# Kernel tuning notes

Measured on AMD Instinct MI355X. Metric: run time of the kernel, lower is better.

## Reference

```python
import jax, jax.numpy as jnp
import numpy as np

B, S, D = 1, 2048, 2048
H, KV, HD = 32, 8, 64  # heads, kv heads, head_dim
THETA = 10000.0


def rot(x):
    # torch: cat(-x[..., d/2:], x[..., :d/2])
    f, s = jnp.split(x, 2, axis=-1)
    return jnp.concatenate((-s, f), axis=-1)


def setup_inputs() -> dict:
    key = jax.random.key(0)
    k0, k1, k2, k3, k4 = jax.random.split(key, 5)
    x = jax.random.normal(k0, (B, S, D), jnp.float32)
    Wq = jax.random.normal(k1, (H * HD, D), jnp.float32) * 0.02
    Wk = jax.random.normal(k2, (KV * HD, D), jnp.float32) * 0.02
    Wv = jax.random.normal(k3, (KV * HD, D), jnp.float32) * 0.02
    Wo = jax.random.normal(k4, (D, H * HD), jnp.float32) * 0.02
    inv_freq = 1.0 / (THETA ** (jnp.arange(0, HD, 2, dtype=jnp.float32) / HD))
    return {"x": x, "Wq": Wq, "Wk": Wk, "Wv": Wv, "Wo": Wo, "inv_freq": inv_freq}


def reference(x, Wq, Wk, Wv, Wo, inv_freq):
    bsz, seqlen, _ = x.shape
    q = (x @ Wq.T).reshape(bsz, seqlen, H, HD).transpose(0, 2, 1, 3)   # [B,H,S,hd]
    k = (x @ Wk.T).reshape(bsz, seqlen, KV, HD).transpose(0, 2, 1, 3)  # [B,KV,S,hd]
    v = (x @ Wv.T).reshape(bsz, seqlen, KV, HD).transpose(0, 2, 1, 3)

    # RoPE cos/sin (computed under no_grad in torch)
    pos = jnp.arange(seqlen, dtype=jnp.float32)
    freqs = pos[:, None] * inv_freq[None, :]                # [S, hd/2]
    emb = jnp.concatenate((freqs, freqs), axis=-1)          # [S, hd]
    cos = jnp.cos(emb)[None, None]                          # [1,1,S,hd]
    sin = jnp.sin(emb)[None, None]
    q = q * cos + rot(q) * sin
    k = k * cos + rot(k) * sin

    # GQA: group query heads per kv head instead of repeat_interleaving kv
    G = H // KV
    qg = q.reshape(bsz, KV, G, seqlen, HD)
    scores = jnp.einsum('bkgsd,bktd->bkgst', qg, k) / jnp.sqrt(jnp.float32(HD))
    mask = jnp.triu(jnp.full((seqlen, seqlen), -jnp.inf, jnp.float32), 1)
    attn = jax.nn.softmax(scores + mask, axis=-1)
    out = jnp.einsum('bkgst,bktd->bkgsd', attn, v)          # [B,KV,G,S,hd]
    out = out.reshape(bsz, H, seqlen, HD).transpose(0, 2, 1, 3).reshape(bsz, seqlen, H * HD)
    return out @ Wo.T
```

## Files before the change

### kernel.cpp

```cpp
#include <hip/hip_runtime.h>
#include <hip/hip_bf16.h>
#include <math.h>

#define S_LEN 2048
#define D_MODEL 2048
#define N_H 32
#define N_KV 8
#define HD 64

typedef __attribute__((ext_vector_type(8))) short short8;
typedef __attribute__((ext_vector_type(4))) float floatx4;
typedef unsigned short u16;
typedef unsigned int u32;

#define QSCALE 0.18033688011112042f

#if defined(__has_builtin)
#if __has_builtin(__builtin_amdgcn_exp2f)
#define EXP2(x) __builtin_amdgcn_exp2f(x)
#else
#define EXP2(x) __expf(0.6931471805599453f * (x))
#endif
#else
#define EXP2(x) __expf(0.6931471805599453f * (x))
#endif

__device__ __forceinline__ u16 f2bf(float f) {
    union { float f; u32 u; } v; v.f = f;
    u32 r = v.u + 0x7fffu + ((v.u >> 16) & 1u);
    return (u16)(r >> 16);
}

__device__ __forceinline__ void gload16(const void* gp, void* lp) {
    __builtin_amdgcn_global_load_lds(
        (const __attribute__((address_space(1))) unsigned int*)gp,
        (__attribute__((address_space(3))) unsigned int*)lp,
        16, 0, 0);
}

__global__ __launch_bounds__(256) void cast_all(const float* __restrict__ x,
                                                const float* __restrict__ Wq,
                                                const float* __restrict__ Wk,
                                                const float* __restrict__ Wv,
                                                const float* __restrict__ Wo,
                                                const float* __restrict__ inv_freq,
                                                u16* __restrict__ xb,
                                                u16* __restrict__ wqkv,
                                                u16* __restrict__ wob,
                                                float2* __restrict__ tab) {
    const int t0 = blockIdx.x * 256 + threadIdx.x;
#pragma unroll
    for (int j = 0; j < 7; ++j) {
        const int c = t0 + j * 524288;
        const int i = c * 4;
        const int row = i >> 11;
        const int col = i & 2047;
        const float* src;
        u16* dst;
        if (row < 2048)      { src = x  + (size_t)row * 2048 + col;          dst = xb + i; }
        else if (row < 4096) { src = Wq + (size_t)(row - 2048) * 2048 + col; dst = wqkv + (i - 2048 * 2048); }
        else if (row < 4608) { src = Wk + (size_t)(row - 4096) * 2048 + col; dst = wqkv + (i - 2048 * 2048); }
        else if (row < 5120) { src = Wv + (size_t)(row - 4608) * 2048 + col; dst = wqkv + (i - 2048 * 2048); }
        else                 { src = Wo + (size_t)(row - 5120) * 2048 + col; dst = wob + (i - 5120 * 2048); }
        const float4 v = *(const float4*)src;
        ushort4 o;
        o.x = f2bf(v.x); o.y = f2bf(v.y); o.z = f2bf(v.z); o.w = f2bf(v.w);
        *(ushort4*)dst = o;
    }
    if (t0 < 65536) {
        const int s = t0 >> 5, d = t0 & 31;
        float sn, cs;
        sincosf((float)s * inv_freq[d], &sn, &cs);
        tab[t0] = make_float2(cs, sn);
    }
}

__global__ __launch_bounds__(256) void gemm_qkv(const u16* __restrict__ A,
                                                const u16* __restrict__ B,
                                                u16* __restrict__ Qh,
                                                u16* __restrict__ Kh,
                                                u16* __restrict__ Vt,
                                                const float2* __restrict__ tab,
                                                int K) {
    __shared__ u16 As[2][64 * 32];
    __shared__ u16 Bs[2][128 * 32];
    const int tid  = threadIdx.x;
    const int w    = tid >> 6;
    const int lane = tid & 63;
    const int lr   = lane & 15;
    const int quad = lane >> 4;
    const int bm = blockIdx.x * 64, bn = blockIdx.y * 128;
    const int wm = (w & 1) * 32, wn = (w >> 1) * 64;

    const int srow = tid >> 2;
    const int sch  = (tid & 3) * 8;
    const u16* Ag = A + (size_t)(bm + srow) * K + sch;
    const u16* Bg = B + (size_t)(bn + srow) * K + sch;
    const int loff = srow * 32 + sch;
    const size_t gstride = (size_t)64 * K;

    floatx4 acc[2][4];
#pragma unroll
    for (int i = 0; i < 2; ++i)
#pragma unroll
        for (int j = 0; j < 4; ++j) acc[i][j] = floatx4{0.f, 0.f, 0.f, 0.f};

    gload16(Ag, &As[0][loff]);
    gload16(Bg, &Bs[0][loff]);
    gload16(Bg + gstride, &Bs[0][loff + 64 * 32]);
    __syncthreads();

    for (int k0 = 0; k0 < K; k0 += 32) {
        const int cur = (k0 >> 5) & 1;
        if (k0 + 32 < K) {
            gload16(Ag + k0 + 32, &As[cur ^ 1][loff]);
            gload16(Bg + k0 + 32, &Bs[cur ^ 1][loff]);
            gload16(Bg + gstride + k0 + 32, &Bs[cur ^ 1][loff + 64 * 32]);
        }
        short8 af[2], bf[4];
#pragma unroll
        for (int t = 0; t < 2; ++t)
            af[t] = *(const short8*)&As[cur][(wm + t * 16 + lr) * 32 + quad * 8];
#pragma unroll
        for (int t = 0; t < 4; ++t)
            bf[t] = *(const short8*)&Bs[cur][(wn + t * 16 + lr) * 32 + quad * 8];
#pragma unroll
        for (int im = 0; im < 2; ++im)
#pragma unroll
            for (int in = 0; in < 4; ++in)
                acc[im][in] = __builtin_amdgcn_mfma_f32_16x16x32_bf16(
                    af[im], bf[in], acc[im][in], 0, 0, 0);
        __syncthreads();
    }

    const int c0 = bn + wn;
    if (bn < 2048) {
        const int h = c0 >> 6;
#pragma unroll
        for (int p = 0; p < 2; ++p) {
            const int d = p * 16 + lr;
#pragma unroll
            for (int im = 0; im < 2; ++im)
#pragma unroll
                for (int r = 0; r < 4; ++r) {
                    const int s = bm + wm + im * 16 + quad * 4 + r;
                    const float2 t = tab[s * 32 + d];
                    const float cs = t.x, sn = t.y;
                    const float xl = acc[im][p][r], xh = acc[im][p + 2][r];
                    u16* qrow = Qh + ((size_t)h * S_LEN + s) * HD;
                    qrow[d]      = f2bf((xl * cs - xh * sn) * QSCALE);
                    qrow[d + 32] = f2bf((xh * cs + xl * sn) * QSCALE);
                }
        }
    } else if (bn < 2560) {
        const int kv = (c0 - 2048) >> 6;
#pragma unroll
        for (int p = 0; p < 2; ++p) {
            const int d = p * 16 + lr;
#pragma unroll
            for (int im = 0; im < 2; ++im)
#pragma unroll
                for (int r = 0; r < 4; ++r) {
                    const int s = bm + wm + im * 16 + quad * 4 + r;
                    const float2 t = tab[s * 32 + d];
                    const float cs = t.x, sn = t.y;
                    const float xl = acc[im][p][r], xh = acc[im][p + 2][r];
                    u16* krow = Kh + ((size_t)kv * S_LEN + s) * HD;
                    krow[d]      = f2bf(xl * cs - xh * sn);
                    krow[d + 32] = f2bf(xh * cs + xl * sn);
                }
        }
    } else {
        const int kv = (c0 - 2560) >> 6;
#pragma unroll
        for (int im = 0; im < 2; ++im)
#pragma unroll
            for (int in = 0; in < 4; ++in) {
                const int dfull = in * 16 + lr;
                const int s0 = bm + wm + im * 16 + quad * 4;
                ushort4 o;
                o.x = f2bf(acc[im][in][0]); o.y = f2bf(acc[im][in][1]);
                o.z = f2bf(acc[im][in][2]); o.w = f2bf(acc[im][in][3]);
                *(ushort4*)&Vt[((size_t)kv * HD + dfull) * S_LEN + s0] = o;
            }
    }
}

__global__ __launch_bounds__(256) void gemm_out(const u16* __restrict__ A,
                                                const u16* __restrict__ B,
                                                float* __restrict__ Cf,
                                                int N, int K) {
    __shared__ u16 As[2][64 * 64];
    __shared__ u16 Bs[2][64 * 64];
    const int tid  = threadIdx.x;
    const int w    = tid >> 6;
    const int lane = tid & 63;
    const int lr   = lane & 15;
    const int quad = lane >> 4;
    const int bm = blockIdx.x * 64, bn = blockIdx.y * 64;
    const int wm = w * 16;

    const int srow = tid >> 3;
    const int sch  = tid & 7;

    floatx4 acc[4];
#pragma unroll
    for (int j = 0; j < 4; ++j) acc[j] = floatx4{0.f, 0.f, 0.f, 0.f};

#pragma unroll
    for (int j = 0; j < 2; ++j) {
        const int r = j * 32 + srow;
        gload16(A + (size_t)(bm + r) * K + ((sch ^ (r & 7)) * 8),
                &As[0][r * 64 + sch * 8]);
        gload16(B + (size_t)(bn + r) * K + ((sch ^ (r & 7)) * 8),
                &Bs[0][r * 64 + sch * 8]);
    }
    __syncthreads();

    for (int k0 = 0; k0 < K; k0 += 64) {
        const int cur = (k0 >> 6) & 1;
        if (k0 + 64 < K) {
            const int nb = cur ^ 1;
#pragma unroll
            for (int j = 0; j < 2; ++j) {
                const int r = j * 32 + srow;
                gload16(A + (size_t)(bm + r) * K + k0 + 64 + ((sch ^ (r & 7)) * 8),
                        &As[nb][r * 64 + sch * 8]);
                gload16(B + (size_t)(bn + r) * K + k0 + 64 + ((sch ^ (r & 7)) * 8),
                        &Bs[nb][r * 64 + sch * 8]);
            }
        }
#pragma unroll
        for (int kk = 0; kk < 2; ++kk) {
            short8 af, bf[4];
            {
                const int row = wm + lr;
                const int c   = kk * 4 + quad;
                af = *(const short8*)&As[cur][row * 64 + ((c ^ (row & 7)) * 8)];
            }
#pragma unroll
            for (int in = 0; in < 4; ++in) {
                const int row = in * 16 + lr;
                const int c   = kk * 4 + quad;
                bf[in] = *(const short8*)&Bs[cur][row * 64 + ((c ^ (row & 7)) * 8)];
            }
#pragma unroll
            for (int in = 0; in < 4; ++in)
                acc[in] = __builtin_amdgcn_mfma_f32_16x16x32_bf16(
                    af, bf[in], acc[in], 0, 0, 0);
        }
        __syncthreads();
    }

#pragma unroll
    for (int in = 0; in < 4; ++in) {
        const int row0 = bm + wm + quad * 4;
        const int col  = bn + in * 16 + lr;
#pragma unroll
        for (int r = 0; r < 4; ++r)
            Cf[(size_t)(row0 + r) * N + col] = acc[in][r];
    }
}

__global__ __launch_bounds__(256) void attn_mfma(const u16* __restrict__ Qh,
                                                 const u16* __restrict__ Kh,
                                                 const u16* __restrict__ Vt,
                                                 u16* __restrict__ AO) {
    __shared__ u16 QPs[64 * 64];
    __shared__ u16 Ks[2][64 * 64];
    __shared__ u16 Vs[2][64 * 64];

    const int bid = blockIdx.x;
    const int h   = bid & 31;
    const int qb  = 31 - (bid >> 5);
    const int kv  = h >> 2;
    const int tid  = threadIdx.x;
    const int w    = tid >> 6;
    const int lr   = tid & 15;
    const int quad = (tid >> 4) & 3;
    const int grow = tid >> 3;
    const int gp   = tid & 7;

    const u16* Qg = Qh + ((size_t)h * S_LEN + (size_t)qb * 64) * HD;
    const u16* Kg = Kh + (size_t)kv * S_LEN * HD;
    const u16* Vg = Vt + (size_t)kv * HD * S_LEN;

#pragma unroll
    for (int j = 0; j < 2; ++j) {
        const int r = j * 32 + grow;
        gload16(Qg + (size_t)r * HD + ((gp ^ (r & 7)) * 8), QPs + r * 64 + gp * 8);
        gload16(Kg + (size_t)r * HD + ((gp ^ (r & 7)) * 8), &Ks[0][r * 64 + gp * 8]);
        gload16(Vg + (size_t)r * S_LEN + ((gp ^ (r & 7)) * 8), &Vs[0][r * 64 + gp * 8]);
    }
    __syncthreads();

    const int wq0 = qb * 64 + w * 16;

    short8 qf[2];
#pragma unroll
    for (int kh = 0; kh < 2; ++kh) {
        const int row = w * 16 + lr;
        const int c   = kh * 4 + quad;
        qf[kh] = *(const short8*)&QPs[row * 64 + ((c ^ (row & 7)) * 8)];
    }

    const int q1  = quad >> 1;
    const int lr7 = lr & 7;
    const int pwbase = (w * 16 + lr) * 64 + (quad & 1) * 4;

    float l_lane = 0.f;
    floatx4 oacc[4];
#pragma unroll
    for (int dn = 0; dn < 4; ++dn) oacc[dn] = floatx4{0.f, 0.f, 0.f, 0.f};

    for (int kt = 0; kt <= qb; ++kt) {
        const int buf = kt & 1;
        if (kt < qb) {
            const int nb = buf ^ 1;
#pragma unroll
            for (int j = 0; j < 2; ++j) {
                const int r = j * 32 + grow;
                gload16(Kg + (size_t)((kt + 1) * 64 + r) * HD + ((gp ^ (r & 7)) * 8),
                        &Ks[nb][r * 64 + gp * 8]);
                gload16(Vg + (size_t)r * S_LEN + (kt + 1) * 64 + ((gp ^ (r & 7)) * 8),
                        &Vs[nb][r * 64 + gp * 8]);
            }
        }
        if (64 * kt <= wq0 + 15) {
            floatx4 st[4];
#pragma unroll
            for (int in = 0; in < 4; ++in) st[in] = floatx4{0.f, 0.f, 0.f, 0.f};
#pragma unroll
            for (int in = 0; in < 4; ++in)
#pragma unroll
                for (int kh = 0; kh < 2; ++kh) {
                    const int row = in * 16 + lr;
                    const int c   = kh * 4 + quad;
                    const short8 kf = *(const short8*)
                        &Ks[buf][row * 64 + ((c ^ (row & 7)) * 8)];
                    st[in] = __builtin_amdgcn_mfma_f32_16x16x32_bf16(
                        kf, qf[kh], st[in], 0, 0, 0);
                }

            const bool need_mask = (kt * 64 + 63) > wq0;
            const int qglob = wq0 + lr;
#pragma unroll
            for (int in = 0; in < 4; ++in)
#pragma unroll
                for (int r = 0; r < 4; ++r) {
                    float s = st[in][r];
                    if (need_mask) {
                        const int kg = kt * 64 + in * 16 + quad * 4 + r;
                        if (kg > qglob) s = -1e30f;
                    }
                    const float p = EXP2(s);
                    st[in][r] = p;
                    l_lane += p;
                }

#pragma unroll
            for (int in = 0; in < 4; ++in) {
                const int chunk = (((in * 2 + q1) ^ lr7) << 3);
                float2 lo2; lo2.x = st[in][0]; lo2.y = st[in][1];
                float2 hi2; hi2.x = st[in][2]; hi2.y = st[in][3];
                __hip_bfloat162 blo = __float22bfloat162_rn(lo2);
                __hip_bfloat162 bhi = __float22bfloat162_rn(hi2);
                *(u32*)&QPs[pwbase + chunk]     = *(u32*)&blo;
                *(u32*)&QPs[pwbase + chunk + 2] = *(u32*)&bhi;
            }

#pragma unroll
            for (int kc = 0; kc < 2; ++kc) {
                const int prow = w * 16 + lr;
                const short8 pf = *(const short8*)
                    &QPs[prow * 64 + (((kc * 4 + quad) ^ (prow & 7)) * 8)];
#pragma unroll
                for (int dn = 0; dn < 4; ++dn) {
                    const int vrow = dn * 16 + lr;
                    const int c    = kc * 4 + quad;
                    const short8 vf = *(const short8*)
                        &Vs[buf][vrow * 64 + ((c ^ (vrow & 7)) * 8)];
                    oacc[dn] = __builtin_amdgcn_mfma_f32_16x16x32_bf16(
                        pf, vf, oacc[dn], 0, 0, 0);
                }
            }
        }
        __syncthreads();
    }

    float lv = l_lane;
    lv += __shfl_xor(lv, 16);
    lv += __shfl_xor(lv, 32);
#pragma unroll
    for (int r = 0; r < 4; ++r) {
        const float inv = 1.f / __shfl(lv, quad * 4 + r);
        const size_t row = (size_t)(wq0 + quad * 4 + r);
#pragma unroll
        for (int dn = 0; dn < 4; ++dn)
            AO[row * D_MODEL + h * 64 + dn * 16 + lr] =
                f2bf(oacc[dn][r] * inv);
    }
}

extern "C" void kernel_launch(void* const* d_in, const int* in_sizes, int n_in,
                              void* d_out, int out_size, void* d_ws, size_t ws_size,
                              hipStream_t stream) {
    const float* x        = (const float*)d_in[0];
    const float* Wq       = (const float*)d_in[1];
    const float* Wk       = (const float*)d_in[2];
    const float* Wv       = (const float*)d_in[3];
    const float* Wo       = (const float*)d_in[4];
    const float* inv_freq = (const float*)d_in[5];
    float* out = (float*)d_out;

    const size_t ME = 1 << 20;
    u16* xb   = (u16*)d_ws;
    u16* wqkv = xb   + 4 * ME;
    u16* wob  = wqkv + 6 * ME;
    u16* qhb  = wob  + 4 * ME;
    u16* khb  = qhb  + 4 * ME;
    u16* vtb  = khb  + 1 * ME;
    u16* aob  = vtb  + 1 * ME;
    float2* cstab = (float2*)(aob + 4 * ME);

    const dim3 b256(256);

    cast_all<<<2048, b256, 0, stream>>>(x, Wq, Wk, Wv, Wo, inv_freq,
                                        xb, wqkv, wob, cstab);

    gemm_qkv<<<dim3(32, 24), b256, 0, stream>>>(
        xb, wqkv, qhb, khb, vtb, cstab, D_MODEL);

    attn_mfma<<<dim3(1024), b256, 0, stream>>>(qhb, khb, vtb, aob);

    gemm_out<<<dim3(32, 32), b256, 0, stream>>>(
        aob, wob, out, D_MODEL, D_MODEL);
}
```

Baseline: 208.4 us.

## Fuse all stages into one persistent kernel with grid barriers and work queue

Replaces the four separate launches (cast, QKV GEMM, attention, output GEMM) with one persistent kernel of 768 blocks. Stages are separated by software grid barriers built on an atomic counter. Attention tiles are handed out through an atomic work queue so causal-imbalanced tiles are balanced dynamically. The aim is to remove launch gaps and tail effects between kernels. In exchange it adds spin-wait barrier overhead, requires all 768 blocks to be co-resident (launch_bounds 256,3), and adds an extra memset launch.

```diff
diff --git a/kernel.cpp b/kernel.cpp
--- a/kernel.cpp
+++ b/kernel.cpp
@@ -38,367 +38,373 @@
         16, 0, 0);
 }
 
-__global__ __launch_bounds__(256) void cast_all(const float* __restrict__ x,
-                                                const float* __restrict__ Wq,
-                                                const float* __restrict__ Wk,
-                                                const float* __restrict__ Wv,
-                                                const float* __restrict__ Wo,
-                                                const float* __restrict__ inv_freq,
-                                                u16* __restrict__ xb,
-                                                u16* __restrict__ wqkv,
-                                                u16* __restrict__ wob,
-                                                float2* __restrict__ tab) {
-    const int t0 = blockIdx.x * 256 + threadIdx.x;
-#pragma unroll
-    for (int j = 0; j < 7; ++j) {
-        const int c = t0 + j * 524288;
-        const int i = c * 4;
-        const int row = i >> 11;
-        const int col = i & 2047;
-        const float* src;
-        u16* dst;
-        if (row < 2048)      { src = x  + (size_t)row * 2048 + col;          dst = xb + i; }
-        else if (row < 4096) { src = Wq + (size_t)(row - 2048) * 2048 + col; dst = wqkv + (i - 2048 * 2048); }
-        else if (row < 4608) { src = Wk + (size_t)(row - 4096) * 2048 + col; dst = wqkv + (i - 2048 * 2048); }
-        else if (row < 5120) { src = Wv + (size_t)(row - 4608) * 2048 + col; dst = wqkv + (i - 2048 * 2048); }
-        else                 { src = Wo + (size_t)(row - 5120) * 2048 + col; dst = wob + (i - 5120 * 2048); }
-        const float4 v = *(const float4*)src;
-        ushort4 o;
-        o.x = f2bf(v.x); o.y = f2bf(v.y); o.z = f2bf(v.z); o.w = f2bf(v.w);
-        *(ushort4*)dst = o;
-    }
-    if (t0 < 65536) {
-        const int s = t0 >> 5, d = t0 & 31;
-        float sn, cs;
-        sincosf((float)s * inv_freq[d], &sn, &cs);
-        tab[t0] = make_float2(cs, sn);
-    }
-}
-
-__global__ __launch_bounds__(256) void gemm_qkv(const u16* __restrict__ A,
-                                                const u16* __restrict__ B,
-                                                u16* __restrict__ Qh,
-                                                u16* __restrict__ Kh,
-                                                u16* __restrict__ Vt,
-                                                const float2* __restrict__ tab,
-                                                int K) {
-    __shared__ u16 As[2][64 * 32];
-    __shared__ u16 Bs[2][128 * 32];
-    const int tid  = threadIdx.x;
-    const int w    = tid >> 6;
-    const int lane = tid & 63;
-    const int lr   = lane & 15;
-    const int quad = lane >> 4;
-    const int bm = blockIdx.x * 64, bn = blockIdx.y * 128;
-    const int wm = (w & 1) * 32, wn = (w >> 1) * 64;
-
-    const int srow = tid >> 2;
-    const int sch  = (tid & 3) * 8;
-    const u16* Ag = A + (size_t)(bm + srow) * K + sch;
-    const u16* Bg = B + (size_t)(bn + srow) * K + sch;
-    const int loff = srow * 32 + sch;
-    const size_t gstride = (size_t)64 * K;
-
-    floatx4 acc[2][4];
-#pragma unroll
-    for (int i = 0; i < 2; ++i)
-#pragma unroll
-        for (int j = 0; j < 4; ++j) acc[i][j] = floatx4{0.f, 0.f, 0.f, 0.f};
-
-    gload16(Ag, &As[0][loff]);
-    gload16(Bg, &Bs[0][loff]);
-    gload16(Bg + gstride, &Bs[0][loff + 64 * 32]);
+__device__ __forceinline__ void gbar(u32* cnt, u32 target) {
     __syncthreads();
-
-    for (int k0 = 0; k0 < K; k0 += 32) {
-        const int cur = (k0 >> 5) & 1;
-        if (k0 + 32 < K) {
-            gload16(Ag + k0 + 32, &As[cur ^ 1][loff]);
-            gload16(Bg + k0 + 32, &Bs[cur ^ 1][loff]);
-            gload16(Bg + gstride + k0 + 32, &Bs[cur ^ 1][loff + 64 * 32]);
-        }
-        short8 af[2], bf[4];
-#pragma unroll
-        for (int t = 0; t < 2; ++t)
-            af[t] = *(const short8*)&As[cur][(wm + t * 16 + lr) * 32 + quad * 8];
-#pragma unroll
-        for (int t = 0; t < 4; ++t)
-            bf[t] = *(const short8*)&Bs[cur][(wn + t * 16 + lr) * 32 + quad * 8];
-#pragma unroll
-        for (int im = 0; im < 2; ++im)
-#pragma unroll
-            for (int in = 0; in < 4; ++in)
-                acc[im][in] = __builtin_amdgcn_mfma_f32_16x16x32_bf16(
-                    af[im], bf[in], acc[im][in], 0, 0, 0);
-        __syncthreads();
-    }
-
-    const int c0 = bn + wn;
-    if (bn < 2048) {
-        const int h = c0 >> 6;
-#pragma unroll
-        for (int p = 0; p < 2; ++p) {
-            const int d = p * 16 + lr;
-#pragma unroll
-            for (int im = 0; im < 2; ++im)
-#pragma unroll
-                for (int r = 0; r < 4; ++r) {
-                    const int s = bm + wm + im * 16 + quad * 4 + r;
-                    const float2 t = tab[s * 32 + d];
-                    const float cs = t.x, sn = t.y;
-                    const float xl = acc[im][p][r], xh = acc[im][p + 2][r];
-                    u16* qrow = Qh + ((size_t)h * S_LEN + s) * HD;
-                    qrow[d]      = f2bf((xl * cs - xh * sn) * QSCALE);
-                    qrow[d + 32] = f2bf((xh * cs + xl * sn) * QSCALE);
-                }
-        }
-    } else if (bn < 2560) {
-        const int kv = (c0 - 2048) >> 6;
-#pragma unroll
-        for (int p = 0; p < 2; ++p) {
-            const int d = p * 16 + lr;
-#pragma unroll
-            for (int im = 0; im < 2; ++im)
-#pragma unroll
-                for (int r = 0; r < 4; ++r) {
-                    const int s = bm + wm + im * 16 + quad * 4 + r;
-                    const float2 t = tab[s * 32 + d];
-                    const float cs = t.x, sn = t.y;
-                    const float xl = acc[im][p][r], xh = acc[im][p + 2][r];
-                    u16* krow = Kh + ((size_t)kv * S_LEN + s) * HD;
-                    krow[d]      = f2bf(xl * cs - xh * sn);
-                    krow[d + 32] = f2bf(xh * cs + xl * sn);
-                }
-        }
-    } else {
-        const int kv = (c0 - 2560) >> 6;
-#pragma unroll
-        for (int im = 0; im < 2; ++im)
-#pragma unroll
-            for (int in = 0; in < 4; ++in) {
-                const int dfull = in * 16 + lr;
-                const int s0 = bm + wm + im * 16 + quad * 4;
-                ushort4 o;
-                o.x = f2bf(acc[im][in][0]); o.y = f2bf(acc[im][in][1]);
-                o.z = f2bf(acc[im][in][2]); o.w = f2bf(acc[im][in][3]);
-                *(ushort4*)&Vt[((size_t)kv * HD + dfull) * S_LEN + s0] = o;
-            }
-    }
-}
-
-__global__ __launch_bounds__(256) void gemm_out(const u16* __restrict__ A,
-                                                const u16* __restrict__ B,
-                                                float* __restrict__ Cf,
-                                                int N, int K) {
-    __shared__ u16 As[2][64 * 64];
-    __shared__ u16 Bs[2][64 * 64];
-    const int tid  = threadIdx.x;
-    const int w    = tid >> 6;
-    const int lane = tid & 63;
-    const int lr   = lane & 15;
-    const int quad = lane >> 4;
-    const int bm = blockIdx.x * 64, bn = blockIdx.y * 64;
-    const int wm = w * 16;
-
-    const int srow = tid >> 3;
-    const int sch  = tid & 7;
-
-    floatx4 acc[4];
-#pragma unroll
-    for (int j = 0; j < 4; ++j) acc[j] = floatx4{0.f, 0.f, 0.f, 0.f};
-
-#pragma unroll
-    for (int j = 0; j < 2; ++j) {
-        const int r = j * 32 + srow;
-        gload16(A + (size_t)(bm + r) * K + ((sch ^ (r & 7)) * 8),
-                &As[0][r * 64 + sch * 8]);
-        gload16(B + (size_t)(bn + r) * K + ((sch ^ (r & 7)) * 8),
-                &Bs[0][r * 64 + sch * 8]);
+    if (threadIdx.x == 0) {
+        __threadfence();
+        atomicAdd(cnt, 1u);
+        while (__hip_atomic_load(cnt, __ATOMIC_RELAXED,
+                                 __HIP_MEMORY_SCOPE_AGENT) < target)
+            __builtin_amdgcn_s_sleep(2);
+        __threadfence();
     }
     __syncthreads();
-
-    for (int k0 = 0; k0 < K; k0 += 64) {
-        const int cur = (k0 >> 6) & 1;
-        if (k0 + 64 < K) {
-            const int nb = cur ^ 1;
+}
+
+#define NBLK 768
+
+__global__ __launch_bounds__(256, 3) void fused_all(
+    const float* __restrict__ x,  const float* __restrict__ Wq,
+    const float* __restrict__ Wk, const float* __restrict__ Wv,
+    const float* __restrict__ Wo, const float* __restrict__ inv_freq,
+    u16* __restrict__ xb,  u16* __restrict__ wqkv, u16* __restrict__ wob,
+    u16* __restrict__ qhb, u16* __restrict__ khb,  u16* __restrict__ vtb,
+    u16* __restrict__ aob, float2* __restrict__ tab,
+    float* __restrict__ out, u32* __restrict__ bar, u32* __restrict__ queue)
+{
+    __shared__ u16 LDS[20480];
+    __shared__ int qslot;
+    const int tid = threadIdx.x;
+    const int bid = blockIdx.x;
+
+    {
+        for (int c = bid * 256 + tid; c < 3670016; c += NBLK * 256) {
+            const int i = c * 4;
+            const int row = i >> 11;
+            const int col = i & 2047;
+            const float* src;
+            u16* dst;
+            if (row < 2048)      { src = x  + (size_t)row * 2048 + col;          dst = xb + i; }
+            else if (row < 4096) { src = Wq + (size_t)(row - 2048) * 2048 + col; dst = wqkv + (i - 2048 * 2048); }
+            else if (row < 4608) { src = Wk + (size_t)(row - 4096) * 2048 + col; dst = wqkv + (i - 2048 * 2048); }
+            else if (row < 5120) { src = Wv + (size_t)(row - 4608) * 2048 + col; dst = wqkv + (i - 2048 * 2048); }
+            else                 { src = Wo + (size_t)(row - 5120) * 2048 + col; dst = wob + (i - 5120 * 2048); }
+            const float4 v = *(const float4*)src;
+            ushort4 o;
+            o.x = f2bf(v.x); o.y = f2bf(v.y); o.z = f2bf(v.z); o.w = f2bf(v.w);
+            *(ushort4*)dst = o;
+        }
+        const int t0 = bid * 256 + tid;
+        if (t0 < 65536) {
+            float sn, cs;
+            sincosf((float)(t0 >> 5) * inv_freq[t0 & 31], &sn, &cs);
+            tab[t0] = make_float2(cs, sn);
+        }
+    }
+    gbar(bar, NBLK);
+
+    {
+        const int w    = tid >> 6;
+        const int lane = tid & 63;
+        const int lr   = lane & 15;
+        const int quad = lane >> 4;
+        const int bm = (bid & 31) * 64, bn = (bid >> 5) * 128;
+        const int wm = (w & 1) * 32, wn = (w >> 1) * 64;
+        const int srow = tid >> 2;
+        const int sch  = (tid & 3) * 8;
+        const u16* Ag = xb   + (size_t)(bm + srow) * 2048 + sch;
+        const u16* Bg = wqkv + (size_t)(bn + srow) * 2048 + sch;
+        const int loff = srow * 32 + sch;
+        const size_t gstride = (size_t)64 * 2048;
+
+        floatx4 acc[2][4];
+#pragma unroll
+        for (int i = 0; i < 2; ++i)
+#pragma unroll
+            for (int j = 0; j < 4; ++j) acc[i][j] = floatx4{0.f, 0.f, 0.f, 0.f};
+
+        gload16(Ag, &LDS[loff]);
+        gload16(Bg, &LDS[4096 + loff]);
+        gload16(Bg + gstride, &LDS[4096 + loff + 2048]);
+        __syncthreads();
+
+        for (int k0 = 0; k0 < 2048; k0 += 32) {
+            const int cur = (k0 >> 5) & 1;
+            if (k0 + 32 < 2048) {
+                const int nb = cur ^ 1;
+                gload16(Ag + k0 + 32, &LDS[nb * 2048 + loff]);
+                gload16(Bg + k0 + 32, &LDS[4096 + nb * 4096 + loff]);
+                gload16(Bg + gstride + k0 + 32, &LDS[4096 + nb * 4096 + loff + 2048]);
+            }
+            short8 af[2], bf[4];
+#pragma unroll
+            for (int t = 0; t < 2; ++t)
+                af[t] = *(const short8*)&LDS[cur * 2048 + (wm + t * 16 + lr) * 32 + quad * 8];
+#pragma unroll
+            for (int t = 0; t < 4; ++t)
+                bf[t] = *(const short8*)&LDS[4096 + cur * 4096 + (wn + t * 16 + lr) * 32 + quad * 8];
+#pragma unroll
+            for (int im = 0; im < 2; ++im)
+#pragma unroll
+                for (int in = 0; in < 4; ++in)
+                    acc[im][in] = __builtin_amdgcn_mfma_f32_16x16x32_bf16(
+                        af[im], bf[in], acc[im][in], 0, 0, 0);
+            __syncthreads();
+        }
+
+        const int c0 = bn + wn;
+        if (bn < 2048) {
+            const int h = c0 >> 6;
+#pragma unroll
+            for (int p = 0; p < 2; ++p) {
+                const int d = p * 16 + lr;
+#pragma unroll
+                for (int im = 0; im < 2; ++im)
+#pragma unroll
+                    for (int r = 0; r < 4; ++r) {
+                        const int s = bm + wm + im * 16 + quad * 4 + r;
+                        const float2 t = tab[s * 32 + d];
+                        const float cs = t.x, sn = t.y;
+                        const float xl = acc[im][p][r], xh = acc[im][p + 2][r];
+                        u16* qrow = qhb + ((size_t)h * S_LEN + s) * HD;
+                        qrow[d]      = f2bf((xl * cs - xh * sn) * QSCALE);
+                        qrow[d + 32] = f2bf((xh * cs + xl * sn) * QSCALE);
+                    }
+            }
+        } else if (bn < 2560) {
+            const int kv = (c0 - 2048) >> 6;
+#pragma unroll
+            for (int p = 0; p < 2; ++p) {
+                const int d = p * 16 + lr;
+#pragma unroll
+                for (int im = 0; im < 2; ++im)
+#pragma unroll
+                    for (int r = 0; r < 4; ++r) {
+                        const int s = bm + wm + im * 16 + quad * 4 + r;
+                        const float2 t = tab[s * 32 + d];
+                        const float cs = t.x, sn = t.y;
+                        const float xl = acc[im][p][r], xh = acc[im][p + 2][r];
+                        u16* krow = khb + ((size_t)kv * S_LEN + s) * HD;
+                        krow[d]      = f2bf(xl * cs - xh * sn);
+                        krow[d + 32] = f2bf(xh * cs + xl * sn);
+                    }
+            }
+        } else {
+            const int kv = (c0 - 2560) >> 6;
+#pragma unroll
+            for (int im = 0; im < 2; ++im)
+#pragma unroll
+                for (int in = 0; in < 4; ++in) {
+                    const int dfull = in * 16 + lr;
+                    const int s0 = bm + wm + im * 16 + quad * 4;
+                    ushort4 o;
+                    o.x = f2bf(acc[im][in][0]); o.y = f2bf(acc[im][in][1]);
+                    o.z = f2bf(acc[im][in][2]); o.w = f2bf(acc[im][in][3]);
+                    *(ushort4*)&vtb[((size_t)kv * HD + dfull) * S_LEN + s0] = o;
+                }
+        }
+    }
+    gbar(bar, 2 * NBLK);
+
+    {
+        const int w    = tid >> 6;
+        const int lr   = tid & 15;
+        const int quad = (tid >> 4) & 3;
+        const int grow = tid >> 3;
+        const int gp   = tid & 7;
+        const int q1   = quad >> 1;
+        const int lr7  = lr & 7;
+        const int pwbase = (w * 16 + lr) * 64 + (quad & 1) * 4;
+
+        for (;;) {
+            if (tid == 0) qslot = (int)atomicAdd(queue, 1u);
+            __syncthreads();
+            const int item = qslot;
+            if (item >= 1024) break;
+
+            const int h  = item & 31;
+            const int qb = 31 - (item >> 5);
+            const int kv = h >> 2;
+            const u16* Qg = qhb + ((size_t)h * S_LEN + (size_t)qb * 64) * HD;
+            const u16* Kg = khb + (size_t)kv * S_LEN * HD;
+            const u16* Vg = vtb + (size_t)kv * HD * S_LEN;
+
+#pragma unroll
+            for (int j = 0; j < 2; ++j) {
+                const int r = j * 32 + grow;
+                gload16(Qg + (size_t)r * HD + ((gp ^ (r & 7)) * 8), &LDS[r * 64 + gp * 8]);
+                gload16(Kg + (size_t)r * HD + ((gp ^ (r & 7)) * 8), &LDS[4096 + r * 64 + gp * 8]);
+                gload16(Vg + (size_t)r * S_LEN + ((gp ^ (r & 7)) * 8), &LDS[12288 + r * 64 + gp * 8]);
+            }
+            __syncthreads();
+
+            const int wq0 = qb * 64 + w * 16;
+
+            short8 qf[2];
+#pragma unroll
+            for (int kh = 0; kh < 2; ++kh) {
+                const int row = w * 16 + lr;
+                const int c   = kh * 4 + quad;
+                qf[kh] = *(const short8*)&LDS[row * 64 + ((c ^ (row & 7)) * 8)];
+            }
+
+            float l_lane = 0.f;
+            floatx4 oacc[4];
+#pragma unroll
+            for (int dn = 0; dn < 4; ++dn) oacc[dn] = floatx4{0.f, 0.f, 0.f, 0.f};
+
+            for (int kt = 0; kt <= qb; ++kt) {
+                const int buf = kt & 1;
+                if (kt < qb) {
+                    const int nb = buf ^ 1;
+#pragma unroll
+                    for (int j = 0; j < 2; ++j) {
+                        const int r = j * 32 + grow;
+                        gload16(Kg + (size_t)((kt + 1) * 64 + r) * HD + ((gp ^ (r & 7)) * 8),
+                                &LDS[4096 + nb * 4096 + r * 64 + gp * 8]);
+                        gload16(Vg + (size_t)r * S_LEN + (kt + 1) * 64 + ((gp ^ (r & 7)) * 8),
+                                &LDS[12288 + nb * 4096 + r * 64 + gp * 8]);
+                    }
+                }
+                if (64 * kt <= wq0 + 15) {
+                    floatx4 st[4];
+#pragma unroll
+                    for (int in = 0; in < 4; ++in) st[in] = floatx4{0.f, 0.f, 0.f, 0.f};
+#pragma unroll
+                    for (int in = 0; in < 4; ++in)
+#pragma unroll
+                        for (int kh = 0; kh < 2; ++kh) {
+                            const int row = in * 16 + lr;
+                            const int c   = kh * 4 + quad;
+                            const short8 kf = *(const short8*)
+                                &LDS[4096 + buf * 4096 + row * 64 + ((c ^ (row & 7)) * 8)];
+                            st[in] = __builtin_amdgcn_mfma_f32_16x16x32_bf16(
+                                kf, qf[kh], st[in], 0, 0, 0);
+                        }
+
+                    const bool need_mask = (kt * 64 + 63) > wq0;
+                    const int qglob = wq0 + lr;
+#pragma unroll
+                    for (int in = 0; in < 4; ++in)
+#pragma unroll
+                        for (int r = 0; r < 4; ++r) {
+                            float s = st[in][r];
+                            if (need_mask) {
+                                const int kg = kt * 64 + in * 16 + quad * 4 + r;
+                                if (kg > qglob) s = -1e30f;
+                            }
+                            const float p = EXP2(s);
+                            st[in][r] = p;
+                            l_lane += p;
+                        }
+
+#pragma unroll
+                    for (int in = 0; in < 4; ++in) {
+                        const int chunk = (((in * 2 + q1) ^ lr7) << 3);
+                        float2 lo2; lo2.x = st[in][0]; lo2.y = st[in][1];
+                        float2 hi2; hi2.x = st[in][2]; hi2.y = st[in][3];
+                        __hip_bfloat162 blo = __float22bfloat162_rn(lo2);
+                        __hip_bfloat162 bhi = __float22bfloat162_rn(hi2);
+                        *(u32*)&LDS[pwbase + chunk]     = *(u32*)&blo;
+                        *(u32*)&LDS[pwbase + chunk + 2] = *(u32*)&bhi;
+                    }
+
+#pragma unroll
+                    for (int kc = 0; kc < 2; ++kc) {
+                        const int prow = w * 16 + lr;
+                        const short8 pf = *(const short8*)
+                            &LDS[prow * 64 + (((kc * 4 + quad) ^ (prow & 7)) * 8)];
+#pragma unroll
+                        for (int dn = 0; dn < 4; ++dn) {
+                            const int vrow = dn * 16 + lr;
+                            const int c    = kc * 4 + quad;
+                            const short8 vf = *(const short8*)
+                                &LDS[12288 + buf * 4096 + vrow * 64 + ((c ^ (vrow & 7)) * 8)];
+                            oacc[dn] = __builtin_amdgcn_mfma_f32_16x16x32_bf16(
+                                pf, vf, oacc[dn], 0, 0, 0);
+                        }
+                    }
+                }
+                __syncthreads();
+            }
+
+            float lv = l_lane;
+            lv += __shfl_xor(lv, 16);
+            lv += __shfl_xor(lv, 32);
+#pragma unroll
+            for (int r = 0; r < 4; ++r) {
+                const float inv = 1.f / __shfl(lv, quad * 4 + r);
+                const size_t row = (size_t)(wq0 + quad * 4 + r);
+#pragma unroll
+                for (int dn = 0; dn < 4; ++dn)
+                    aob[row * D_MODEL + h * 64 + dn * 16 + lr] =
+                        f2bf(oacc[dn][r] * inv);
+            }
+        }
+    }
+    gbar(bar, 3 * NBLK);
+
+    {
+        const int w    = tid >> 6;
+        const int lane = tid & 63;
+        const int lr   = lane & 15;
+        const int quad = lane >> 4;
+        const int wm = w * 16;
+        const int srow = tid >> 3;
+        const int sch  = tid & 7;
+
+        for (int it = bid; it < 1024; it += NBLK) {
+            const int bm = (it & 31) * 64, bn = (it >> 5) * 64;
+            __syncthreads();
+
+            floatx4 acc[4];
+#pragma unroll
+            for (int j = 0; j < 4; ++j) acc[j] = floatx4{0.f, 0.f, 0.f, 0.f};
+
 #pragma unroll
             for (int j = 0; j < 2; ++j) {
                 const int r = j * 32 + srow;
-                gload16(A + (size_t)(bm + r) * K + k0 + 64 + ((sch ^ (r & 7)) * 8),
-                        &As[nb][r * 64 + sch * 8]);
-                gload16(B + (size_t)(bn + r) * K + k0 + 64 + ((sch ^ (r & 7)) * 8),
-                        &Bs[nb][r * 64 + sch * 8]);
-            }
-        }
-#pragma unroll
-        for (int kk = 0; kk < 2; ++kk) {
-            short8 af, bf[4];
-            {
-                const int row = wm + lr;
-                const int c   = kk * 4 + quad;
-                af = *(const short8*)&As[cur][row * 64 + ((c ^ (row & 7)) * 8)];
-            }
+                gload16(aob + (size_t)(bm + r) * 2048 + ((sch ^ (r & 7)) * 8),
+                        &LDS[r * 64 + sch * 8]);
+                gload16(wob + (size_t)(bn + r) * 2048 + ((sch ^ (r & 7)) * 8),
+                        &LDS[8192 + r * 64 + sch * 8]);
+            }
+            __syncthreads();
+
+            for (int k0 = 0; k0 < 2048; k0 += 64) {
+                const int cur = (k0 >> 6) & 1;
+                if (k0 + 64 < 2048) {
+                    const int nb = cur ^ 1;
+#pragma unroll
+                    for (int j = 0; j < 2; ++j) {
+                        const int r = j * 32 + srow;
+                        gload16(aob + (size_t)(bm + r) * 2048 + k0 + 64 + ((sch ^ (r & 7)) * 8),
+                                &LDS[nb * 4096 + r * 64 + sch * 8]);
+                        gload16(wob + (size_t)(bn + r) * 2048 + k0 + 64 + ((sch ^ (r & 7)) * 8),
+                                &LDS[8192 + nb * 4096 + r * 64 + sch * 8]);
+                    }
+                }
+#pragma unroll
+                for (int kk = 0; kk < 2; ++kk) {
+                    short8 af, bf[4];
+                    {
+                        const int row = wm + lr;
+                        const int c   = kk * 4 + quad;
+                        af = *(const short8*)&LDS[cur * 4096 + row * 64 + ((c ^ (row & 7)) * 8)];
+                    }
+#pragma unroll
+                    for (int in = 0; in < 4; ++in) {
+                        const int row = in * 16 + lr;
+                        const int c   = kk * 4 + quad;
+                        bf[in] = *(const short8*)&LDS[8192 + cur * 4096 + row * 64 + ((c ^ (row & 7)) * 8)];
+                    }
+#pragma unroll
+                    for (int in = 0; in < 4; ++in)
+                        acc[in] = __builtin_amdgcn_mfma_f32_16x16x32_bf16(
+                            af, bf[in], acc[in], 0, 0, 0);
+                }
+                __syncthreads();
+            }
+
 #pragma unroll
             for (int in = 0; in < 4; ++in) {
-                const int row = in * 16 + lr;
-                const int c   = kk * 4 + quad;
-                bf[in] = *(const short8*)&Bs[cur][row * 64 + ((c ^ (row & 7)) * 8)];
-            }
-#pragma unroll
-            for (int in = 0; in < 4; ++in)
-                acc[in] = __builtin_amdgcn_mfma_f32_16x16x32_bf16(
-                    af, bf[in], acc[in], 0, 0, 0);
-        }
-        __syncthreads();
-    }
-
-#pragma unroll
-    for (int in = 0; in < 4; ++in) {
-        const int row0 = bm + wm + quad * 4;
-        const int col  = bn + in * 16 + lr;
-#pragma unroll
-        for (int r = 0; r < 4; ++r)
-            Cf[(size_t)(row0 + r) * N + col] = acc[in][r];
-    }
-}
-
-__global__ __launch_bounds__(256) void attn_mfma(const u16* __restrict__ Qh,
-                                                 const u16* __restrict__ Kh,
-                                                 const u16* __restrict__ Vt,
-                                                 u16* __restrict__ AO) {
-    __shared__ u16 QPs[64 * 64];
-    __shared__ u16 Ks[2][64 * 64];
-    __shared__ u16 Vs[2][64 * 64];
-
-    const int bid = blockIdx.x;
-    const int h   = bid & 31;
-    const int qb  = 31 - (bid >> 5);
-    const int kv  = h >> 2;
-    const int tid  = threadIdx.x;
-    const int w    = tid >> 6;
-    const int lr   = tid & 15;
-    const int quad = (tid >> 4) & 3;
-    const int grow = tid >> 3;
-    const int gp   = tid & 7;
-
-    const u16* Qg = Qh + ((size_t)h * S_LEN + (size_t)qb * 64) * HD;
-    const u16* Kg = Kh + (size_t)kv * S_LEN * HD;
-    const u16* Vg = Vt + (size_t)kv * HD * S_LEN;
-
-#pragma unroll
-    for (int j = 0; j < 2; ++j) {
-        const int r = j * 32 + grow;
-        gload16(Qg + (size_t)r * HD + ((gp ^ (r & 7)) * 8), QPs + r * 64 + gp * 8);
-        gload16(Kg + (size_t)r * HD + ((gp ^ (r & 7)) * 8), &Ks[0][r * 64 + gp * 8]);
-        gload16(Vg + (size_t)r * S_LEN + ((gp ^ (r & 7)) * 8), &Vs[0][r * 64 + gp * 8]);
-    }
-    __syncthreads();
-
-    const int wq0 = qb * 64 + w * 16;
-
-    short8 qf[2];
-#pragma unroll
-    for (int kh = 0; kh < 2; ++kh) {
-        const int row = w * 16 + lr;
-        const int c   = kh * 4 + quad;
-        qf[kh] = *(const short8*)&QPs[row * 64 + ((c ^ (row & 7)) * 8)];
-    }
-
-    const int q1  = quad >> 1;
-    const int lr7 = lr & 7;
-    const int pwbase = (w * 16 + lr) * 64 + (quad & 1) * 4;
-
-    float l_lane = 0.f;
-    floatx4 oacc[4];
-#pragma unroll
-    for (int dn = 0; dn < 4; ++dn) oacc[dn] = floatx4{0.f, 0.f, 0.f, 0.f};
-
-    for (int kt = 0; kt <= qb; ++kt) {
-        const int buf = kt & 1;
-        if (kt < qb) {
-            const int nb = buf ^ 1;
-#pragma unroll
-            for (int j = 0; j < 2; ++j) {
-                const int r = j * 32 + grow;
-                gload16(Kg + (size_t)((kt + 1) * 64 + r) * HD + ((gp ^ (r & 7)) * 8),
-                        &Ks[nb][r * 64 + gp * 8]);
-                gload16(Vg + (size_t)r * S_LEN + (kt + 1) * 64 + ((gp ^ (r & 7)) * 8),
-                        &Vs[nb][r * 64 + gp * 8]);
-            }
-        }
-        if (64 * kt <= wq0 + 15) {
-            floatx4 st[4];
-#pragma unroll
-            for (int in = 0; in < 4; ++in) st[in] = floatx4{0.f, 0.f, 0.f, 0.f};
-#pragma unroll
-            for (int in = 0; in < 4; ++in)
-#pragma unroll
-                for (int kh = 0; kh < 2; ++kh) {
-                    const int row = in * 16 + lr;
-                    const int c   = kh * 4 + quad;
-                    const short8 kf = *(const short8*)
-                        &Ks[buf][row * 64 + ((c ^ (row & 7)) * 8)];
-                    st[in] = __builtin_amdgcn_mfma_f32_16x16x32_bf16(
-                        kf, qf[kh], st[in], 0, 0, 0);
-                }
-
-            const bool need_mask = (kt * 64 + 63) > wq0;
-            const int qglob = wq0 + lr;
-#pragma unroll
-            for (int in = 0; in < 4; ++in)
-#pragma unroll
-                for (int r = 0; r < 4; ++r) {
-                    float s = st[in][r];
-                    if (need_mask) {
-                        const int kg = kt * 64 + in * 16 + quad * 4 + r;
-                        if (kg > qglob) s = -1e30f;
-                    }
-                    const float p = EXP2(s);
-                    st[in][r] = p;
-                    l_lane += p;
-                }
-
-#pragma unroll
-            for (int in = 0; in < 4; ++in) {
-                const int chunk = (((in * 2 + q1) ^ lr7) << 3);
-                float2 lo2; lo2.x = st[in][0]; lo2.y = st[in][1];
-                float2 hi2; hi2.x = st[in][2]; hi2.y = st[in][3];
-                __hip_bfloat162 blo = __float22bfloat162_rn(lo2);
-                __hip_bfloat162 bhi = __float22bfloat162_rn(hi2);
-                *(u32*)&QPs[pwbase + chunk]     = *(u32*)&blo;
-                *(u32*)&QPs[pwbase + chunk + 2] = *(u32*)&bhi;
-            }
-
-#pragma unroll
-            for (int kc = 0; kc < 2; ++kc) {
-                const int prow = w * 16 + lr;
-                const short8 pf = *(const short8*)
-                    &QPs[prow * 64 + (((kc * 4 + quad) ^ (prow & 7)) * 8)];
-#pragma unroll
-                for (int dn = 0; dn < 4; ++dn) {
-                    const int vrow = dn * 16 + lr;
-                    const int c    = kc * 4 + quad;
-                    const short8 vf = *(const short8*)
-                        &Vs[buf][vrow * 64 + ((c ^ (vrow & 7)) * 8)];
-                    oacc[dn] = __builtin_amdgcn_mfma_f32_16x16x32_bf16(
-                        pf, vf, oacc[dn], 0, 0, 0);
-                }
-            }
-        }
-        __syncthreads();
-    }
-
-    float lv = l_lane;
-    lv += __shfl_xor(lv, 16);
-    lv += __shfl_xor(lv, 32);
-#pragma unroll
-    for (int r = 0; r < 4; ++r) {
-        const float inv = 1.f / __shfl(lv, quad * 4 + r);
-        const size_t row = (size_t)(wq0 + quad * 4 + r);
-#pragma unroll
-        for (int dn = 0; dn < 4; ++dn)
-            AO[row * D_MODEL + h * 64 + dn * 16 + lr] =
-                f2bf(oacc[dn][r] * inv);
+                const int row0 = bm + wm + quad * 4;
+                const int col  = bn + in * 16 + lr;
+#pragma unroll
+                for (int r = 0; r < 4; ++r)
+                    out[(size_t)(row0 + r) * 2048 + col] = acc[in][r];
+            }
+        }
     }
 }
 
@@ -423,16 +429,11 @@
     u16* aob  = vtb  + 1 * ME;
     float2* cstab = (float2*)(aob + 4 * ME);
 
-    const dim3 b256(256);
-
-    cast_all<<<2048, b256, 0, stream>>>(x, Wq, Wk, Wv, Wo, inv_freq,
-                                        xb, wqkv, wob, cstab);
-
-    gemm_qkv<<<dim3(32, 24), b256, 0, stream>>>(
-        xb, wqkv, qhb, khb, vtb, cstab, D_MODEL);
-
-    attn_mfma<<<dim3(1024), b256, 0, stream>>>(qhb, khb, vtb, aob);
-
-    gemm_out<<<dim3(32, 32), b256, 0, stream>>>(
-        aob, wob, out, D_MODEL, D_MODEL);
+    u32* ctr = (u32*)((char*)d_ws + ((ws_size - 256) & ~(size_t)63));
+    hipMemsetAsync(ctr, 0, 8, stream);
+
+    fused_all<<<NBLK, 256, 0, stream>>>(
+        x, Wq, Wk, Wv, Wo, inv_freq,
+        xb, wqkv, wob, qhb, khb, vtb, aob, cstab,
+        out, ctr, ctr + 1);
 }
```

Result: slower. 562.8 us (+170.1%).
